# Optimization experiments

Measured on AMD Instinct MI355X. Metric: run time of the kernel, lower is better.

The kernel has to match this reference:

```python
import jax, jax.numpy as jnp
import numpy as np
from jax import lax

WINDOW_SIZE = 11
SIGMA = 1.5
CHANNEL = 1
C1 = 0.01 ** 2
C2 = 0.03 ** 2
EPS = 1e-8


def _gaussian_window(window_size, sigma, channel):
    coords = jnp.arange(window_size, dtype=jnp.float32) - window_size // 2
    g = jnp.exp(-coords ** 2 / (2.0 * sigma ** 2))
    g = g / g.sum()
    w2d = jnp.outer(g, g)  # [ws, ws]
    # depthwise conv kernel, OIHW with I=1 (groups=channel)
    return jnp.broadcast_to(w2d[None, None], (channel, 1, window_size, window_size))


def _blur(x, window, channel):
    # depthwise 2D conv, SAME padding (padding = ws//2 for odd ws)
    return lax.conv_general_dilated(
        x, window, window_strides=(1, 1), padding="SAME",
        feature_group_count=channel,
        dimension_numbers=("NCHW", "OIHW", "NCHW"))


def setup_inputs() -> dict:
    key = jax.random.key(0)
    k1, k2 = jax.random.split(key)
    B, C, H, W = 32, CHANNEL, 512, 512
    pred = jax.random.uniform(k1, (B, C, H, W), dtype=jnp.float32)
    target = jax.random.uniform(k2, (B, C, H, W), dtype=jnp.float32)
    window = _gaussian_window(WINDOW_SIZE, SIGMA, CHANNEL)
    return {"pred": pred, "target": target, "window": window}


def reference(pred, target, window):
    channel = pred.shape[1]
    mu_p = _blur(pred, window, channel)
    mu_t = _blur(target, window, channel)
    mu_p_sq = mu_p ** 2
    mu_t_sq = mu_t ** 2
    mu_pt = mu_p * mu_t
    sigma_p_sq = _blur(pred ** 2, window, channel) - mu_p_sq
    sigma_t_sq = _blur(target ** 2, window, channel) - mu_t_sq
    sigma_pt = _blur(pred * target, window, channel) - mu_pt
    sigma_p_sq = jnp.maximum(sigma_p_sq, 0.0)
    sigma_t_sq = jnp.maximum(sigma_t_sq, 0.0)
    numerator = (2.0 * mu_pt + C1) * (2.0 * sigma_pt + C2)
    denominator = (mu_p_sq + mu_t_sq + C1) * (sigma_p_sq + sigma_t_sq + C2)
    ssim_map = numerator / (denominator + EPS)
    return 1.0 - jnp.mean(ssim_map)
```

## Files before the change

kernel.cpp:

```cpp
#include <hip/hip_runtime.h>

typedef _Float16 f16x2 __attribute__((ext_vector_type(2)));
typedef _Float16 f16x4 __attribute__((ext_vector_type(4)));
typedef _Float16 f16x8 __attribute__((ext_vector_type(8)));
typedef float    f32x4 __attribute__((ext_vector_type(4)));

#define NBLK 8192

__device__ __forceinline__ f16x2 pkrtz(float a, float b) {
    return __builtin_bit_cast(f16x2, __builtin_amdgcn_cvt_pkrtz(a, b));
}

__global__ __launch_bounds__(256, 5)
void ssim_fused(const float* __restrict__ pred,
                const float* __restrict__ targ,
                const float* __restrict__ win,
                float* __restrict__ partial)
{
    __shared__ __align__(16) _Float16 rawT[4 * 80 * 32];
    __shared__ __align__(16) _Float16 vbuf[4 * 16 * 88];
    __shared__ float gw[16];
    __shared__ float wsum[4];

    const int tid  = threadIdx.x;
    const int lane = tid & 63;
    const int wv   = tid >> 6;
    const int bid  = blockIdx.x;
    const int b    = bid >> 8;
    const int rem  = bid & 255;
    const int ty   = rem >> 3;
    const int tx   = rem & 7;
    const int x0g  = tx * 64 - 5;
    const int y0g  = ty * 16 - 5;

    if (tid < 11) {
        float s = 0.f;
        #pragma unroll
        for (int j = 0; j < 11; ++j) s += win[tid * 11 + j];
        gw[tid] = s;
    }

    const float* pb = pred + (size_t)b * (512 * 512);
    const float* tb = targ + (size_t)b * (512 * 512);
    const bool interior = (tx >= 1) & (tx <= 6) & (ty >= 1) & (ty <= 30);

    if (tid < 240) {
        const int x  = tid % 80;
        const int r0 = tid / 80;
        const int gx = x0g + x;
        const int sw = (x >> 1) & 7;
        const bool xok = (unsigned)gx < 512u;
        _Float16* rb = &rawT[x * 32];
        for (int qy = r0; qy < 8; qy += 3) {
            const int gy = y0g + qy * 4;
            float p0, p1, p2, p3, t0, t1, t2, t3;
            if (interior) {
                const float* pp = pb + (size_t)gy * 512 + gx;
                const float* tp = tb + (size_t)gy * 512 + gx;
                p0 = pp[0]; p1 = pp[512]; p2 = pp[1024]; p3 = pp[1536];
                t0 = tp[0]; t1 = tp[512]; t2 = tp[1024]; t3 = tp[1536];
            } else {
                p0 = p1 = p2 = p3 = t0 = t1 = t2 = t3 = 0.f;
                if (xok) {
                    const float* pp = pb + (size_t)gy * 512 + gx;
                    const float* tp = tb + (size_t)gy * 512 + gx;
                    if ((unsigned)(gy    ) < 512u) { p0 = pp[0];    t0 = tp[0];    }
                    if ((unsigned)(gy + 1) < 512u) { p1 = pp[512];  t1 = tp[512];  }
                    if ((unsigned)(gy + 2) < 512u) { p2 = pp[1024]; t2 = tp[1024]; }
                    if ((unsigned)(gy + 3) < 512u) { p3 = pp[1536]; t3 = tp[1536]; }
                }
            }
            const int off = (qy ^ sw) << 2;
            union { f16x2 h2[2]; f16x4 v; } u;
            u.h2[0] = pkrtz(p0, p1);
            u.h2[1] = pkrtz(p2, p3);
            *(f16x4*)&rb[off] = u.v;
            u.h2[0] = pkrtz(t0, t1);
            u.h2[1] = pkrtz(t2, t3);
            *(f16x4*)&rb[2560 + off] = u.v;
            u.h2[0] = pkrtz(fmaf(p0, p0, t0 * t0), fmaf(p1, p1, t1 * t1));
            u.h2[1] = pkrtz(fmaf(p2, p2, t2 * t2), fmaf(p3, p3, t3 * t3));
            *(f16x4*)&rb[5120 + off] = u.v;
            u.h2[0] = pkrtz(p0 * t0, p1 * t1);
            u.h2[1] = pkrtz(p2 * t2, p3 * t3);
            *(f16x4*)&rb[7680 + off] = u.v;
        }
    }
    __syncthreads();

    const int mrow = lane & 15;
    const int quad = lane >> 4;
    f16x8 afr;
    #pragma unroll
    for (int j = 0; j < 8; ++j) {
        const int d = quad * 8 + j - mrow;
        afr[j] = (d >= 0 && d < 11) ? (_Float16)gw[d] : (_Float16)0.f;
    }
    const f32x4 z4 = {0.f, 0.f, 0.f, 0.f};

    const int swr = mrow >> 1;
    #pragma unroll
    for (int c = 0; c < 5; ++c) {
        const int x = c * 16 + mrow;
        const _Float16* base = &rawT[wv * 2560 + x * 32];
        union { f16x4 h[2]; f16x8 v; } bu;
        bu.h[0] = *(const f16x4*)&base[((2 * quad    ) ^ swr) << 2];
        bu.h[1] = *(const f16x4*)&base[((2 * quad + 1) ^ swr) << 2];
        const f32x4 dv = __builtin_amdgcn_mfma_f32_16x16x32_f16(afr, bu.v, z4, 0, 0, 0);
        #pragma unroll
        for (int r = 0; r < 4; ++r)
            vbuf[wv * 1408 + (quad * 4 + r) * 88 + x] = (_Float16)dv[r];
    }
    __syncthreads();

    float lsum = 0.f;
    {
        const int X0 = wv * 16;
        f32x4 dq[4];
        #pragma unroll
        for (int pl = 0; pl < 4; ++pl) {
            const f16x8 bv = *(const f16x8*)&vbuf[pl * 1408 + mrow * 88 + X0 + quad * 8];
            dq[pl] = __builtin_amdgcn_mfma_f32_16x16x32_f16(afr, bv, z4, 0, 0, 0);
        }
        #pragma unroll
        for (int r = 0; r < 4; ++r) {
            const float mp = dq[0][r], mt = dq[1][r];
            const float sv = dq[2][r], qv = dq[3][r];
            const float mp2 = mp * mp, mt2 = mt * mt, mpt = mp * mt;
            const float sig = fmaxf(sv - mp2 - mt2, 0.f);
            const float cv  = qv - mpt;
            const float num = (2.f * mpt + 1e-4f) * (2.f * cv + 9e-4f);
            const float den = (mp2 + mt2 + 1e-4f) * (sig + 9e-4f);
            lsum += num * __builtin_amdgcn_rcpf(den + 1e-8f);
        }
    }

    #pragma unroll
    for (int off = 32; off > 0; off >>= 1)
        lsum += __shfl_down(lsum, off, 64);
    if (lane == 0) wsum[wv] = lsum;
    __syncthreads();
    if (tid == 0)
        partial[bid] = wsum[0] + wsum[1] + wsum[2] + wsum[3];
}

__global__ __launch_bounds__(256)
void ssim_reduce(const float* __restrict__ partial, float* __restrict__ out)
{
    __shared__ double ws[4];
    double s = 0.0;
    const f32x4* p4 = (const f32x4*)partial;
    for (int i = threadIdx.x; i < NBLK / 4; i += 256) {
        const f32x4 v = p4[i];
        s += (double)v[0] + (double)v[1] + (double)v[2] + (double)v[3];
    }
    #pragma unroll
    for (int off = 32; off > 0; off >>= 1)
        s += __shfl_down(s, off, 64);
    if ((threadIdx.x & 63) == 0) ws[threadIdx.x >> 6] = s;
    __syncthreads();
    if (threadIdx.x == 0) {
        const double tot = ws[0] + ws[1] + ws[2] + ws[3];
        out[0] = (float)(1.0 - tot / 8388608.0);
    }
}

extern "C" void kernel_launch(void* const* d_in, const int* in_sizes, int n_in,
                              void* d_out, int out_size, void* d_ws, size_t ws_size,
                              hipStream_t stream)
{
    const float* pred = (const float*)d_in[0];
    const float* targ = (const float*)d_in[1];
    const float* win  = (const float*)d_in[2];
    float* out     = (float*)d_out;
    float* partial = (float*)d_ws;

    ssim_fused<<<NBLK, 256, 0, stream>>>(pred, targ, win, partial);
    ssim_reduce<<<1, 256, 0, stream>>>(partial, out);
}
```

Baseline: 116.5 us.

## Use 64x32 tiles with float4 loads and compute squared planes in MFMA stage

Doubles the tile height to 32 rows, which halves the block count and reduces redundant halo loads (halo now 8 on each side, aligned for float4). Global loads become float4 vectors instead of scalar strided loads. Only the pred and target planes are staged in LDS, and each wave builds its own plane (p, t, p²+t², p·t) in f16 registers before the vertical MFMA. The trade-offs are lower occupancy (launch bounds 3), more LDS per block, and squares now computed in f16, which changes precision.

New measurement: 120.1 us. 1.03x slower.

```diff
diff --git a/kernel.cpp b/kernel.cpp
--- a/kernel.cpp
+++ b/kernel.cpp
@@ -5,20 +5,20 @@
 typedef _Float16 f16x8 __attribute__((ext_vector_type(8)));
 typedef float    f32x4 __attribute__((ext_vector_type(4)));
 
-#define NBLK 8192
+#define NBLK 4096
 
 __device__ __forceinline__ f16x2 pkrtz(float a, float b) {
     return __builtin_bit_cast(f16x2, __builtin_amdgcn_cvt_pkrtz(a, b));
 }
 
-__global__ __launch_bounds__(256, 5)
+__global__ __launch_bounds__(256, 3)
 void ssim_fused(const float* __restrict__ pred,
                 const float* __restrict__ targ,
                 const float* __restrict__ win,
                 float* __restrict__ partial)
 {
-    __shared__ __align__(16) _Float16 rawT[4 * 80 * 32];
-    __shared__ __align__(16) _Float16 vbuf[4 * 16 * 88];
+    __shared__ __align__(16) _Float16 rawT[2 * 80 * 64];
+    __shared__ __align__(16) _Float16 vbuf[4 * 32 * 88];
     __shared__ float gw[16];
     __shared__ float wsum[4];
 
@@ -26,12 +26,12 @@
     const int lane = tid & 63;
     const int wv   = tid >> 6;
     const int bid  = blockIdx.x;
-    const int b    = bid >> 8;
-    const int rem  = bid & 255;
+    const int b    = bid >> 7;
+    const int rem  = bid & 127;
     const int ty   = rem >> 3;
     const int tx   = rem & 7;
-    const int x0g  = tx * 64 - 5;
-    const int y0g  = ty * 16 - 5;
+    const int x0g  = tx * 64 - 8;
+    const int y0g  = ty * 32 - 8;
 
     if (tid < 11) {
         float s = 0.f;
@@ -42,48 +42,62 @@
 
     const float* pb = pred + (size_t)b * (512 * 512);
     const float* tb = targ + (size_t)b * (512 * 512);
-    const bool interior = (tx >= 1) & (tx <= 6) & (ty >= 1) & (ty <= 30);
+    const bool interior = (tx >= 1) & (tx <= 6) & (ty >= 1) & (ty <= 14);
 
     if (tid < 240) {
-        const int x  = tid % 80;
-        const int r0 = tid / 80;
-        const int gx = x0g + x;
-        const int sw = (x >> 1) & 7;
-        const bool xok = (unsigned)gx < 512u;
-        _Float16* rb = &rawT[x * 32];
-        for (int qy = r0; qy < 8; qy += 3) {
-            const int gy = y0g + qy * 4;
-            float p0, p1, p2, p3, t0, t1, t2, t3;
-            if (interior) {
-                const float* pp = pb + (size_t)gy * 512 + gx;
-                const float* tp = tb + (size_t)gy * 512 + gx;
-                p0 = pp[0]; p1 = pp[512]; p2 = pp[1024]; p3 = pp[1536];
-                t0 = tp[0]; t1 = tp[512]; t2 = tp[1024]; t3 = tp[1536];
-            } else {
-                p0 = p1 = p2 = p3 = t0 = t1 = t2 = t3 = 0.f;
-                if (xok) {
-                    const float* pp = pb + (size_t)gy * 512 + gx;
-                    const float* tp = tb + (size_t)gy * 512 + gx;
-                    if ((unsigned)(gy    ) < 512u) { p0 = pp[0];    t0 = tp[0];    }
-                    if ((unsigned)(gy + 1) < 512u) { p1 = pp[512];  t1 = tp[512];  }
-                    if ((unsigned)(gy + 2) < 512u) { p2 = pp[1024]; t2 = tp[1024]; }
-                    if ((unsigned)(gy + 3) < 512u) { p3 = pp[1536]; t3 = tp[1536]; }
+        const int xi = tid % 20;
+        const int qy = tid / 20;
+        const int lx = xi * 4;
+        const int gx = x0g + lx;
+        const int gy = y0g + qy * 4;
+        float4 pr[4], tr[4];
+        if (interior) {
+            const float* pp = pb + (size_t)gy * 512 + gx;
+            const float* tp = tb + (size_t)gy * 512 + gx;
+            #pragma unroll
+            for (int r = 0; r < 4; ++r) {
+                pr[r] = *(const float4*)(pp + r * 512);
+                tr[r] = *(const float4*)(tp + r * 512);
+            }
+        } else {
+            const bool xin = (gx >= 0) & (gx + 3 < 512);
+            #pragma unroll
+            for (int r = 0; r < 4; ++r) {
+                const int gyr = gy + r;
+                const bool yok = (unsigned)gyr < 512u;
+                if (yok && xin) {
+                    pr[r] = *(const float4*)(pb + (size_t)gyr * 512 + gx);
+                    tr[r] = *(const float4*)(tb + (size_t)gyr * 512 + gx);
+                } else {
+                    float4 pz = {0.f, 0.f, 0.f, 0.f};
+                    float4 tz = {0.f, 0.f, 0.f, 0.f};
+                    if (yok) {
+                        #pragma unroll
+                        for (int e = 0; e < 4; ++e) {
+                            const int gxe = gx + e;
+                            if ((unsigned)gxe < 512u) {
+                                pz[e] = pb[(size_t)gyr * 512 + gxe];
+                                tz[e] = tb[(size_t)gyr * 512 + gxe];
+                            }
+                        }
+                    }
+                    pr[r] = pz; tr[r] = tz;
                 }
             }
-            const int off = (qy ^ sw) << 2;
+        }
+        #pragma unroll
+        for (int e = 0; e < 4; ++e) {
+            const int x  = lx + e;
+            const int sw = (x >> 1) & 7;
+            const int sc = (qy & 8) | ((qy & 7) ^ sw);
+            _Float16* col = &rawT[x * 64 + sc * 4];
             union { f16x2 h2[2]; f16x4 v; } u;
-            u.h2[0] = pkrtz(p0, p1);
-            u.h2[1] = pkrtz(p2, p3);
-            *(f16x4*)&rb[off] = u.v;
-            u.h2[0] = pkrtz(t0, t1);
-            u.h2[1] = pkrtz(t2, t3);
-            *(f16x4*)&rb[2560 + off] = u.v;
-            u.h2[0] = pkrtz(fmaf(p0, p0, t0 * t0), fmaf(p1, p1, t1 * t1));
-            u.h2[1] = pkrtz(fmaf(p2, p2, t2 * t2), fmaf(p3, p3, t3 * t3));
-            *(f16x4*)&rb[5120 + off] = u.v;
-            u.h2[0] = pkrtz(p0 * t0, p1 * t1);
-            u.h2[1] = pkrtz(p2 * t2, p3 * t3);
-            *(f16x4*)&rb[7680 + off] = u.v;
+            u.h2[0] = pkrtz(pr[0][e], pr[1][e]);
+            u.h2[1] = pkrtz(pr[2][e], pr[3][e]);
+            *(f16x4*)col = u.v;
+            u.h2[0] = pkrtz(tr[0][e], tr[1][e]);
+            u.h2[1] = pkrtz(tr[2][e], tr[3][e]);
+            *(f16x4*)(col + 5120) = u.v;
         }
     }
     __syncthreads();
@@ -93,45 +107,68 @@
     f16x8 afr;
     #pragma unroll
     for (int j = 0; j < 8; ++j) {
-        const int d = quad * 8 + j - mrow;
+        const int d = quad * 8 + j - mrow - 3;
         afr[j] = (d >= 0 && d < 11) ? (_Float16)gw[d] : (_Float16)0.f;
     }
     const f32x4 z4 = {0.f, 0.f, 0.f, 0.f};
-
     const int swr = mrow >> 1;
+
     #pragma unroll
     for (int c = 0; c < 5; ++c) {
         const int x = c * 16 + mrow;
-        const _Float16* base = &rawT[wv * 2560 + x * 32];
-        union { f16x4 h[2]; f16x8 v; } bu;
-        bu.h[0] = *(const f16x4*)&base[((2 * quad    ) ^ swr) << 2];
-        bu.h[1] = *(const f16x4*)&base[((2 * quad + 1) ^ swr) << 2];
-        const f32x4 dv = __builtin_amdgcn_mfma_f32_16x16x32_f16(afr, bu.v, z4, 0, 0, 0);
-        #pragma unroll
-        for (int r = 0; r < 4; ++r)
-            vbuf[wv * 1408 + (quad * 4 + r) * 88 + x] = (_Float16)dv[r];
+        const _Float16* bp = &rawT[x * 64];
+        #pragma unroll
+        for (int h = 0; h < 2; ++h) {
+            const int sc0 = h * 4 + 2 * quad;
+            const int sc1 = sc0 + 1;
+            const int o0  = (((sc0 & 8) | ((sc0 & 7) ^ swr))) << 2;
+            const int o1  = (((sc1 & 8) | ((sc1 & 7) ^ swr))) << 2;
+            union { f16x4 q[2]; f16x8 v; } pu, tu;
+            if (wv != 1) {
+                pu.q[0] = *(const f16x4*)&bp[o0];
+                pu.q[1] = *(const f16x4*)&bp[o1];
+            }
+            if (wv != 0) {
+                tu.q[0] = *(const f16x4*)&bp[5120 + o0];
+                tu.q[1] = *(const f16x4*)&bp[5120 + o1];
+            }
+            f16x8 frag;
+            if      (wv == 0) frag = pu.v;
+            else if (wv == 1) frag = tu.v;
+            else if (wv == 2) frag = pu.v * pu.v + tu.v * tu.v;
+            else              frag = pu.v * tu.v;
+            const f32x4 dv = __builtin_amdgcn_mfma_f32_16x16x32_f16(afr, frag, z4, 0, 0, 0);
+            _Float16* vb = &vbuf[wv * 2816 + (h * 16 + quad * 4) * 88 + x];
+            #pragma unroll
+            for (int r = 0; r < 4; ++r)
+                vb[r * 88] = (_Float16)dv[r];
+        }
     }
     __syncthreads();
 
     float lsum = 0.f;
     {
         const int X0 = wv * 16;
-        f32x4 dq[4];
-        #pragma unroll
-        for (int pl = 0; pl < 4; ++pl) {
-            const f16x8 bv = *(const f16x8*)&vbuf[pl * 1408 + mrow * 88 + X0 + quad * 8];
-            dq[pl] = __builtin_amdgcn_mfma_f32_16x16x32_f16(afr, bv, z4, 0, 0, 0);
-        }
-        #pragma unroll
-        for (int r = 0; r < 4; ++r) {
-            const float mp = dq[0][r], mt = dq[1][r];
-            const float sv = dq[2][r], qv = dq[3][r];
-            const float mp2 = mp * mp, mt2 = mt * mt, mpt = mp * mt;
-            const float sig = fmaxf(sv - mp2 - mt2, 0.f);
-            const float cv  = qv - mpt;
-            const float num = (2.f * mpt + 1e-4f) * (2.f * cv + 9e-4f);
-            const float den = (mp2 + mt2 + 1e-4f) * (sig + 9e-4f);
-            lsum += num * __builtin_amdgcn_rcpf(den + 1e-8f);
+        #pragma unroll
+        for (int yh = 0; yh < 2; ++yh) {
+            f32x4 dq[4];
+            #pragma unroll
+            for (int pl = 0; pl < 4; ++pl) {
+                const f16x8 bv = *(const f16x8*)
+                    &vbuf[pl * 2816 + (yh * 16 + mrow) * 88 + X0 + quad * 8];
+                dq[pl] = __builtin_amdgcn_mfma_f32_16x16x32_f16(afr, bv, z4, 0, 0, 0);
+            }
+            #pragma unroll
+            for (int r = 0; r < 4; ++r) {
+                const float mp = dq[0][r], mt = dq[1][r];
+                const float sv = dq[2][r], qv = dq[3][r];
+                const float mp2 = mp * mp, mt2 = mt * mt, mpt = mp * mt;
+                const float sig = fmaxf(sv - mp2 - mt2, 0.f);
+                const float cv  = qv - mpt;
+                const float num = (2.f * mpt + 1e-4f) * (2.f * cv + 9e-4f);
+                const float den = (mp2 + mt2 + 1e-4f) * (sig + 9e-4f);
+                lsum += num * __builtin_amdgcn_rcpf(den + 1e-8f);
+            }
         }
     }
 
```
